# Performance work log

Hardware: AMD Instinct MI355X
Metric: run time of the kernel (lower is better)

## Reference

```python
import jax, jax.numpy as jnp
import numpy as np

HEAD_NUM = 16
MASK_FILL = 100000.0  # source uses +1e5 on masked entries (not -inf)


def setup_inputs() -> dict:
    key = jax.random.key(0)
    k1, k2, k3, k4, k5 = jax.random.split(key, 5)
    B, S, E = 2, 2048, 1024
    scale = 0.02
    return {
        "x": jax.random.normal(k1, (B, S, E), dtype=jnp.float32),
        "W_atten": jax.random.normal(k2, (E, 3 * E), dtype=jnp.float32) * scale,
        "b_atten": jax.random.normal(k3, (3 * E,), dtype=jnp.float32) * scale,
        "W_proj": jax.random.normal(k4, (E, E), dtype=jnp.float32) * scale,
        "b_proj": jax.random.normal(k5, (E,), dtype=jnp.float32) * scale,
    }


def reference(x, W_atten, b_atten, W_proj, b_proj):
    B, S, E = x.shape
    H = HEAD_NUM
    hd = E // H
    # QKV projection: [B, S, 3E]
    qkv = x @ W_atten + b_atten
    # reshape [B, S, H, 3*hd] -> [B, H, S, 3*hd], chunk into q,k,v [B,H,S,hd]
    qkv = jnp.transpose(qkv.reshape(B, S, H, 3 * hd), (0, 2, 1, 3))
    q, k, v = jnp.split(qkv, 3, axis=-1)
    # raw scores, NO 1/sqrt(dk) scaling (faithful to source)
    w = jnp.einsum("bhqd,bhkd->bhqk", q, k)
    # causal mask applied as w*mask + (1-mask)*1e5 (faithful to source)
    mask = jnp.tril(jnp.ones((S, S), dtype=w.dtype))
    w = w * mask + (1.0 - mask) * MASK_FILL
    # softmax over dim=1 == HEAD axis (faithful to source quirk)
    w = jax.nn.softmax(w, axis=1)
    # attn_drop: identity in eval mode
    a = jnp.einsum("bhqk,bhkd->bhqd", w, v)  # [B,H,S,hd]
    a = jnp.transpose(a, (0, 2, 1, 3)).reshape(B, S, E)
    h = a @ W_proj + b_proj
    # resi_drop: identity in eval mode
    return h
```

## Files before the change

### kernel.cpp

```cpp
#include <hip/hip_runtime.h>

#define DI __device__ __forceinline__

typedef __attribute__((ext_vector_type(8))) short s16x8;
typedef __attribute__((ext_vector_type(4))) short s16x4;
typedef __attribute__((ext_vector_type(4))) float f32x4;

DI unsigned short f2bf(float f){
  unsigned u = __float_as_uint(f);
  u = (u + 0x7FFFu + ((u >> 16) & 1u)) >> 16;
  return (unsigned short)u;
}
DI float bf2f(unsigned short h){
  return __uint_as_float(((unsigned)h) << 16);
}

DI void gll16(const void* g, void* l){
  __builtin_amdgcn_global_load_lds((const __attribute__((address_space(1))) void*)g,
                                   (__attribute__((address_space(3))) void*)l, 16, 0, 0);
}

__global__ void cvt_kernel(const float* __restrict__ in, unsigned short* __restrict__ out, int n8){
  int i = blockIdx.x * blockDim.x + threadIdx.x;
  if (i >= n8) return;
  const float4* p = (const float4*)in + (size_t)i * 2;
  float4 a = p[0], b = p[1];
  s16x8 o;
  o[0] = (short)f2bf(a.x); o[1] = (short)f2bf(a.y); o[2] = (short)f2bf(a.z); o[3] = (short)f2bf(a.w);
  o[4] = (short)f2bf(b.x); o[5] = (short)f2bf(b.y); o[6] = (short)f2bf(b.z); o[7] = (short)f2bf(b.w);
  ((s16x8*)out)[i] = o;
}

__global__ void transpose_cvt(const float* __restrict__ in, unsigned short* __restrict__ out, int R, int C){
  __shared__ float t[32][33];
  int c0 = blockIdx.x * 32, r0 = blockIdx.y * 32;
  int tx = threadIdx.x, ty = threadIdx.y;
  #pragma unroll
  for (int i = 0; i < 4; i++)
    t[ty + i*8][tx] = in[(size_t)(r0 + ty + i*8) * C + c0 + tx];
  __syncthreads();
  #pragma unroll
  for (int i = 0; i < 4; i++)
    out[(size_t)(c0 + ty + i*8) * R + r0 + tx] = f2bf(t[tx][ty + i*8]);
}

template<int MODE, int BM>
__launch_bounds__(256)
__global__ void gemm_kernel(const unsigned short* __restrict__ A,
                            const unsigned short* __restrict__ Wt,
                            const float* __restrict__ bias,
                            int N,
                            unsigned short* __restrict__ qb,
                            unsigned short* __restrict__ kb,
                            unsigned short* __restrict__ vt,
                            float* __restrict__ out)
{
  constexpr int MI = BM / 32;
  constexpr int AC = BM / 32;
  const int K = 1024;
  __shared__ unsigned short As[BM * 64];
  __shared__ unsigned short Bs[128 * 64];
  int m0 = blockIdx.y * BM, n0 = blockIdx.x * 128;
  int tid = threadIdx.x;
  int lane = tid & 63, w = tid >> 6;
  int row_l = lane & 15, kgrp = lane >> 4;
  int wm = (w >> 1) * (MI * 16), wn = (w & 1) * 64;

  const unsigned short* asrc[AC];
  const unsigned short* bsrc[4];
  int ldsoA[AC], ldsoB[4];
  int chunk = (lane & 7) ^ (lane >> 3);
  #pragma unroll
  for (int c4 = 0; c4 < AC; c4++){
    int r = c4*32 + w*8 + (lane >> 3);
    asrc[c4] = A + (size_t)(m0 + r) * K + chunk*8;
    ldsoA[c4] = (c4*32 + w*8) * 64;
  }
  #pragma unroll
  for (int c4 = 0; c4 < 4; c4++){
    int r = c4*32 + w*8 + (lane >> 3);
    bsrc[c4] = Wt + (size_t)(n0 + r) * K + chunk*8;
    ldsoB[c4] = (c4*32 + w*8) * 64;
  }
  int eA[MI], eB[4];
  #pragma unroll
  for (int i = 0; i < MI; i++){
    int ra = wm + i*16 + row_l;
    eA[i] = (ra*64 + kgrp*8) ^ ((ra & 7) << 3);
  }
  #pragma unroll
  for (int i = 0; i < 4; i++){
    int rb = wn + i*16 + row_l;
    eB[i] = (rb*64 + kgrp*8) ^ ((rb & 7) << 3);
  }

  f32x4 acc[MI][4];
  #pragma unroll
  for (int i = 0; i < MI; i++)
    #pragma unroll
    for (int j = 0; j < 4; j++)
      acc[i][j] = (f32x4){0.f, 0.f, 0.f, 0.f};

  for (int k0 = 0; k0 < K; k0 += 64){
    #pragma unroll
    for (int c4 = 0; c4 < AC; c4++)
      gll16(asrc[c4] + k0, (void*)(As + ldsoA[c4]));
    #pragma unroll
    for (int c4 = 0; c4 < 4; c4++)
      gll16(bsrc[c4] + k0, (void*)(Bs + ldsoB[c4]));
    __syncthreads();
    #pragma unroll
    for (int kc = 0; kc < 2; kc++){
      s16x8 af[MI], bfr[4];
      #pragma unroll
      for (int mi = 0; mi < MI; mi++)
        af[mi] = *(const s16x8*)&As[eA[mi] ^ (kc*32)];
      #pragma unroll
      for (int ni = 0; ni < 4; ni++)
        bfr[ni] = *(const s16x8*)&Bs[eB[ni] ^ (kc*32)];
      #pragma unroll
      for (int mi = 0; mi < MI; mi++)
        #pragma unroll
        for (int ni = 0; ni < 4; ni++)
          acc[mi][ni] = __builtin_amdgcn_mfma_f32_16x16x32_bf16(af[mi], bfr[ni], acc[mi][ni], 0, 0, 0);
    }
    __syncthreads();
  }

  #pragma unroll
  for (int mi = 0; mi < MI; mi++){
    #pragma unroll
    for (int ni = 0; ni < 4; ni++){
      #pragma unroll
      for (int j = 0; j < 4; j++){
        int gr = m0 + wm + mi*16 + kgrp*4 + j;
        int gc = n0 + wn + ni*16 + row_l;
        float v = acc[mi][ni][j] + bias[gc];
        if (MODE == 0){
          int h = gc / 192, cc = gc % 192;
          int b = gr >> 11, s = gr & 2047;
          unsigned short bv = f2bf(v);
          if (cc < 64){
            qb[(size_t)gr * 1024 + h*64 + cc] = bv;
          } else if (cc < 128){
            int d = cc - 64; int kt = s >> 6, kk = s & 63;
            kb[(size_t)((b*16 + h)*32 + kt) * 4096 + ((kk*64 + d) ^ ((kk & 7) << 3))] = bv;
          } else {
            int d = cc - 128; int kt = s >> 6, kk = s & 63;
            vt[(size_t)((b*16 + h)*32 + kt) * 4096 + ((d*64 + kk) ^ ((d & 7) << 3))] = bv;
          }
        } else {
          out[(size_t)gr * N + gc] = v;
        }
      }
    }
  }
}

__global__ void sufv_kernel(const unsigned short* __restrict__ vt, float* __restrict__ sufv){
  __shared__ float tot[4][64];
  int bh = blockIdx.x;
  int tid = threadIdx.x;
  int tq = tid >> 6, d = tid & 63;
  const unsigned short* base = vt + (size_t)bh * 32 * 4096;
  float s[8];
  float run = 0.f;
  for (int j = 7; j >= 0; j--){
    int t = tq*8 + j;
    float rs = 0.f;
    #pragma unroll
    for (int c = 0; c < 8; c++){
      int idx = (d*64 + c*8) ^ ((d & 7) << 3);
      s16x8 v = *(const s16x8*)&base[(size_t)t*4096 + idx];
      #pragma unroll
      for (int e = 0; e < 8; e++) rs += bf2f((unsigned short)v[e]);
    }
    run += rs; s[j] = run;
  }
  tot[tq][d] = run;
  __syncthreads();
  float carry = 0.f;
  for (int t2 = tq+1; t2 < 4; t2++) carry += tot[t2][d];
  #pragma unroll
  for (int j = 0; j < 8; j++)
    sufv[((size_t)bh*33 + tq*8 + j)*64 + d] = s[j] + carry;
  if (tid < 64) sufv[((size_t)bh*33 + 32)*64 + tid] = 0.f;
}

__launch_bounds__(256)
__global__ void dpass_kernel(const unsigned short* __restrict__ qbuf,
                             const unsigned short* __restrict__ kb,
                             float* __restrict__ invDQ)
{
  __shared__ unsigned short Kst[4][4096];
  int bid = blockIdx.x;
  int blk = (bid & 7) * 132 + (bid >> 3);
  int b = blk / 528, t = blk % 528;
  int kt = (int)(32.5f - sqrtf(1056.25f - 2.f*t));
  while (kt*(65-kt)/2 > t) kt--;
  while ((kt+1)*(64-kt)/2 <= t) kt++;
  int qt = kt + (t - kt*(65-kt)/2);

  int tid = threadIdx.x, lane = tid & 63, w = tid >> 6;
  int row_l = lane & 15, kgrp = lane >> 4;

  const unsigned short* ktb = kb + ((size_t)(b*16)*32 + kt) * 4096;
  int sgoff = (w*128 + lane)*8;

  auto stage = [&](int hh, int buf){
    const unsigned short* src = ktb + (size_t)hh * 131072;
    gll16(src + sgoff,       (void*)(&Kst[buf][0] + w*1024));
    gll16(src + sgoff + 512, (void*)(&Kst[buf][0] + w*1024 + 512));
  };

  int e0[4];
  #pragma unroll
  for (int ks = 0; ks < 4; ks++){
    int row = ks*16 + row_l;
    e0[ks] = (row*64 + kgrp*8) ^ ((row & 7) << 3);
  }

  stage(0, 0);
  stage(1, 1);

  f32x4 esum[4];
  #pragma unroll
  for (int ks = 0; ks < 4; ks++) esum[ks] = (f32x4){0.f,0.f,0.f,0.f};

  const unsigned short* qrow_p = qbuf + (size_t)(b*2048 + qt*64 + w*16 + row_l) * 1024;
  s16x8 qf0 = *(const s16x8*)&qrow_p[kgrp*8];
  s16x8 qf1 = *(const s16x8*)&qrow_p[32 + kgrp*8];

  for (int h = 0; h < 16; h++){
    s16x8 qn0, qn1;
    if (h < 15){
      qn0 = *(const s16x8*)&qrow_p[(h+1)*64 + kgrp*8];
      qn1 = *(const s16x8*)&qrow_p[(h+1)*64 + 32 + kgrp*8];
    }
    if (h + 2 < 16) stage(h+2, (h+2) & 3);
    __builtin_amdgcn_sched_barrier(0);
    if (h < 14)      asm volatile("s_waitcnt vmcnt(8)" ::: "memory");
    else if (h < 15) asm volatile("s_waitcnt vmcnt(6)" ::: "memory");
    else             asm volatile("s_waitcnt vmcnt(2)" ::: "memory");
    __builtin_amdgcn_sched_barrier(0);
    __builtin_amdgcn_s_barrier();
    __builtin_amdgcn_sched_barrier(0);

    const unsigned short* kl = &Kst[h & 3][0];
    #pragma unroll
    for (int ks = 0; ks < 4; ks++){
      s16x8 a0 = *(const s16x8*)&kl[e0[ks]];
      s16x8 a1 = *(const s16x8*)&kl[e0[ks] ^ 32];
      f32x4 sc = __builtin_amdgcn_mfma_f32_16x16x32_bf16(a0, qf0, (f32x4){0.f,0.f,0.f,0.f}, 0, 0, 0);
      sc = __builtin_amdgcn_mfma_f32_16x16x32_bf16(a1, qf1, sc, 0, 0, 0);
      #pragma unroll
      for (int j = 0; j < 4; j++) esum[ks][j] += __expf(sc[j]);
    }
    if (h < 15){ qf0 = qn0; qf1 = qn1; }
  }

  int qcol = qt*64 + w*16 + row_l;
  float* dst = invDQ + (size_t)b*4194304 + (size_t)qcol*2048 + kt*64 + kgrp*4;
  #pragma unroll
  for (int ks = 0; ks < 4; ks++){
    f32x4 rv;
    #pragma unroll
    for (int j = 0; j < 4; j++) rv[j] = 1.f / esum[ks][j];
    *(f32x4*)&dst[ks*16] = rv;
  }
}

__launch_bounds__(256)
__global__ void pv_kernel(const unsigned short* __restrict__ qbuf,
                          const unsigned short* __restrict__ kb,
                          const unsigned short* __restrict__ vt,
                          const float* __restrict__ invDQ,
                          const float* __restrict__ sufv,
                          unsigned short* __restrict__ ab,
                          float* __restrict__ pb)
{
  __shared__ unsigned short Kst[2][4096];
  __shared__ unsigned short Vst[2][4096];
  __shared__ unsigned short Wsh[4][1152];

  int blk = ((blockIdx.x & 7) << 7) + (blockIdx.x >> 3);
  int b = blk >> 9;
  int r = blk & 511;
  int h = r >> 5;
  int r2 = r & 31;
  int i = r2 >> 1, half = r2 & 1;
  int qsm = i, qbig = 31 - i;

  int tid = threadIdx.x, lane = tid & 63, w = tid >> 6;
  int row_l = lane & 15, kgrp = lane >> 4;

  const unsigned short* KT = kb + (size_t)((b*16 + h)*32) * 4096;
  const unsigned short* VT = vt + (size_t)((b*16 + h)*32) * 4096;
  int sgoff = (w*128 + lane)*8;
  unsigned short* Wsw = &Wsh[w][0];

  int eK[4];
  #pragma unroll
  for (int ks = 0; ks < 4; ks++){
    int row = ks*16 + row_l;
    eK[ks] = (row*64 + kgrp*8) ^ ((row & 7) << 3);
  }

  auto stage = [&](int kt, int buf){
    gll16(KT + (size_t)kt*4096 + sgoff,       (void*)(&Kst[buf][0] + w*1024));
    gll16(KT + (size_t)kt*4096 + sgoff + 512, (void*)(&Kst[buf][0] + w*1024 + 512));
    gll16(VT + (size_t)kt*4096 + sgoff,       (void*)(&Vst[buf][0] + w*1024));
    gll16(VT + (size_t)kt*4096 + sgoff + 512, (void*)(&Vst[buf][0] + w*1024 + 512));
  };

  auto run = [&](int qt, int k0t, int k1t, int mode){
    int q0 = qt * 64;
    int qv = q0 + w*16 + row_l;
    const unsigned short* qrow_p = qbuf + (size_t)(b*2048 + qv) * 1024 + h*64;
    s16x8 qf0 = *(const s16x8*)&qrow_p[kgrp*8];
    s16x8 qf1 = *(const s16x8*)&qrow_p[32 + kgrp*8];
    const float* ivrow = invDQ + (size_t)b*4194304 + (size_t)qv*2048 + kgrp*4;

    f32x4 pvv[4];
    #pragma unroll
    for (int d = 0; d < 4; d++) pvv[d] = (f32x4){0.f,0.f,0.f,0.f};

    __syncthreads();
    stage(k0t, 0);
    f32x4 inxt[4];
    #pragma unroll
    for (int ks = 0; ks < 4; ks++) inxt[ks] = *(const f32x4*)&ivrow[k0t*64 + ks*16];

    for (int kt = k0t; kt < k1t; kt++){
      int bufc = (kt - k0t) & 1;
      bool nx = (kt + 1 < k1t);
      __builtin_amdgcn_s_barrier();
      if (nx) stage(kt+1, bufc ^ 1);
      f32x4 icur[4];
      #pragma unroll
      for (int ks = 0; ks < 4; ks++) icur[ks] = inxt[ks];
      if (nx){
        #pragma unroll
        for (int ks = 0; ks < 4; ks++) inxt[ks] = *(const f32x4*)&ivrow[(kt+1)*64 + ks*16];
      }
      __builtin_amdgcn_sched_barrier(0);
      if (nx) asm volatile("s_waitcnt vmcnt(12)" ::: "memory");
      else    asm volatile("s_waitcnt vmcnt(4)" ::: "memory");
      __builtin_amdgcn_sched_barrier(0);
      __builtin_amdgcn_s_barrier();
      __builtin_amdgcn_sched_barrier(0);

      const unsigned short* kl = &Kst[bufc][0];
      const unsigned short* vl = &Vst[bufc][0];
      f32x4 sc[4];
      #pragma unroll
      for (int ks = 0; ks < 4; ks++){
        s16x8 a0 = *(const s16x8*)&kl[eK[ks]];
        s16x8 a1 = *(const s16x8*)&kl[eK[ks] ^ 32];
        sc[ks] = __builtin_amdgcn_mfma_f32_16x16x32_bf16(a0, qf0, (f32x4){0.f,0.f,0.f,0.f}, 0, 0, 0);
        sc[ks] = __builtin_amdgcn_mfma_f32_16x16x32_bf16(a1, qf1, sc[ks], 0, 0, 0);
      }
      int kbase = kt*64 + kgrp*4;
      #pragma unroll
      for (int ks = 0; ks < 4; ks++){
        #pragma unroll
        for (int j = 0; j < 4; j++){
          float e = __expf(sc[ks][j]);
          sc[ks][j] = (kbase + ks*16 + j > qv) ? 0.0625f : e * icur[ks][j];
        }
        unsigned lo, hi;
        asm("v_cvt_pk_bf16_f32 %0, %1, %2" : "=v"(lo) : "v"(sc[ks][0]), "v"(sc[ks][1]));
        asm("v_cvt_pk_bf16_f32 %0, %1, %2" : "=v"(hi) : "v"(sc[ks][2]), "v"(sc[ks][3]));
        uint2 pk2; pk2.x = lo; pk2.y = hi;
        *(uint2*)&Wsw[row_l*72 + ks*16 + kgrp*4] = pk2;
      }
      #pragma unroll
      for (int kc = 0; kc < 2; kc++){
        s16x8 af = *(const s16x8*)&Wsw[row_l*72 + kc*32 + kgrp*8];
        #pragma unroll
        for (int dq = 0; dq < 4; dq++){
          s16x8 vf = *(const s16x8*)&vl[eK[dq] ^ (kc*32)];
          pvv[dq] = __builtin_amdgcn_mfma_f32_16x16x32_bf16(af, vf, pvv[dq], 0, 0, 0);
        }
      }
    }

    if (mode == 0){
      int tsuf = qt + 1;
      #pragma unroll
      for (int dq = 0; dq < 4; dq++){
        int d = dq*16 + row_l;
        float suf = sufv[((size_t)(b*16 + h)*33 + tsuf)*64 + d];
        #pragma unroll
        for (int j = 0; j < 4; j++){
          int qo = q0 + w*16 + kgrp*4 + j;
          ab[(size_t)(b*2048 + qo)*1024 + h*64 + d] = f2bf(pvv[dq][j] + 0.0625f * suf);
        }
      }
    } else {
      float* pr = pb + ((size_t)((b*16 + h)*16 + i)*2 + (mode - 1)) * 4096;
      #pragma unroll
      for (int dq = 0; dq < 4; dq++){
        int d = dq*16 + row_l;
        #pragma unroll
        for (int j = 0; j < 4; j++)
          pr[(w*16 + kgrp*4 + j)*64 + d] = pvv[dq][j];
      }
    }
  };

  if (half == 0){
    run(qsm, 0, i + 1, 0);
    run(qbig, 0, 16 - i, 1);
  } else {
    run(qbig, 16 - i, 32 - i, 2);
  }
}

__global__ void reduce_kernel(const float* __restrict__ pb,
                              const float* __restrict__ sufv,
                              unsigned short* __restrict__ ab)
{
  int blk = blockIdx.x;
  int b = blk >> 8, rr = blk & 255;
  int h = rr >> 4, i = rr & 15;
  int qbig = 31 - i, tsuf = 32 - i;
  int t = threadIdx.x;
  int q = t >> 2, dbase = (t & 3) * 16;
  const float* p0 = pb + ((size_t)((b*16 + h)*16 + i)*2 + 0)*4096 + q*64 + dbase;
  const float* p1 = p0 + 4096;
  const float* sf = sufv + ((size_t)(b*16 + h)*33 + tsuf)*64 + dbase;
  unsigned short* op = ab + (size_t)(b*2048 + qbig*64 + q)*1024 + h*64 + dbase;
  #pragma unroll
  for (int e = 0; e < 4; e++){
    float4 a = *(const float4*)(p0 + e*4);
    float4 bb = *(const float4*)(p1 + e*4);
    float4 s = *(const float4*)(sf + e*4);
    unsigned short o[4];
    o[0] = f2bf(a.x + bb.x + 0.0625f * s.x);
    o[1] = f2bf(a.y + bb.y + 0.0625f * s.y);
    o[2] = f2bf(a.z + bb.z + 0.0625f * s.z);
    o[3] = f2bf(a.w + bb.w + 0.0625f * s.w);
    *(s16x4*)(op + e*4) = *(s16x4*)o;
  }
}

extern "C" void kernel_launch(void* const* d_in, const int* in_sizes, int n_in,
                              void* d_out, int out_size, void* d_ws, size_t ws_size,
                              hipStream_t stream) {
  (void)in_sizes; (void)n_in; (void)out_size; (void)ws_size;
  const float* x  = (const float*)d_in[0];
  const float* Wa = (const float*)d_in[1];
  const float* ba = (const float*)d_in[2];
  const float* Wp = (const float*)d_in[3];
  const float* bp = (const float*)d_in[4];
  float* out = (float*)d_out;

  char* ws = (char*)d_ws;
  size_t off = 0;
  auto alloc = [&](size_t bytes) -> void* {
    void* p = ws + off;
    off += (bytes + 255) & ~(size_t)255;
    return p;
  };
  float* pbuf          = (float*)alloc((size_t)16*1024*1024);
  unsigned short* xb   = (unsigned short*)((char*)pbuf);
  unsigned short* WaT  = (unsigned short*)((char*)pbuf + (size_t)4096*1024*2);
  unsigned short* WpT  = (unsigned short*)alloc((size_t)1024*1024*2);
  unsigned short* qbuf = (unsigned short*)alloc((size_t)4096*1024*2);
  unsigned short* ktile= (unsigned short*)alloc((size_t)4096*1024*2);
  unsigned short* vtile= (unsigned short*)alloc((size_t)4096*1024*2);
  unsigned short* abuf = (unsigned short*)alloc((size_t)4096*1024*2);
  float* invDQ         = (float*)alloc((size_t)2*2048*2048*4);
  float* sufv          = (float*)alloc((size_t)32*33*64*4);

  cvt_kernel<<<2048, 256, 0, stream>>>(x, xb, 4096*1024/8);
  transpose_cvt<<<dim3(3072/32, 1024/32), dim3(32, 8), 0, stream>>>(Wa, WaT, 1024, 3072);
  transpose_cvt<<<dim3(1024/32, 1024/32), dim3(32, 8), 0, stream>>>(Wp, WpT, 1024, 1024);

  gemm_kernel<0,128><<<dim3(24, 32), 256, 0, stream>>>(xb, WaT, ba, 3072, qbuf, ktile, vtile, nullptr);

  sufv_kernel<<<32, 256, 0, stream>>>(vtile, sufv);

  dpass_kernel<<<1056, 256, 0, stream>>>(qbuf, ktile, invDQ);

  pv_kernel<<<1024, 256, 0, stream>>>(qbuf, ktile, vtile, invDQ, sufv, abuf, pbuf);

  reduce_kernel<<<512, 256, 0, stream>>>(pbuf, sufv, abuf);

  gemm_kernel<1,64><<<dim3(1024/128, 4096/64), 256, 0, stream>>>(abuf, WpT, bp, 1024, nullptr, nullptr, nullptr, out);
}
```

Before: 182.8 us.

## Store inverse denominators in bf16, use exp2 with prescaled Q, deepen K prefetch

Q is prescaled by log2(e) in the QKV GEMM epilogue so both attention kernels can use the raw v_exp_f32 (exp2) instruction instead of __expf. The per-(q,k) inverse-denominator buffer goes from fp32 to bf16, halving its write and read traffic. pv_kernel gains a triple-buffered K stage with split K/V staging and a two-step-ahead prefetch of the inverse values, skips causal masking on tiles off the diagonal, adds s_setprio around the MFMA blocks, and sets a 3-blocks-per-SM launch bound. The bf16 inverse factors lose precision, and the extra LDS and register limit may affect occupancy.

```diff
diff --git a/kernel.cpp b/kernel.cpp
--- a/kernel.cpp
+++ b/kernel.cpp
@@ -14,11 +14,14 @@
 DI float bf2f(unsigned short h){
   return __uint_as_float(((unsigned)h) << 16);
 }
+DI float exp2i(float x){ float r; asm("v_exp_f32 %0, %1" : "=v"(r) : "v"(x)); return r; }
 
 DI void gll16(const void* g, void* l){
   __builtin_amdgcn_global_load_lds((const __attribute__((address_space(1))) void*)g,
                                    (__attribute__((address_space(3))) void*)l, 16, 0, 0);
 }
+
+#define VMCNT(n) asm volatile("s_waitcnt vmcnt(" #n ")" ::: "memory")
 
 __global__ void cvt_kernel(const float* __restrict__ in, unsigned short* __restrict__ out, int n8){
   int i = blockIdx.x * blockDim.x + threadIdx.x;
@@ -139,15 +142,14 @@
         if (MODE == 0){
           int h = gc / 192, cc = gc % 192;
           int b = gr >> 11, s = gr & 2047;
-          unsigned short bv = f2bf(v);
           if (cc < 64){
-            qb[(size_t)gr * 1024 + h*64 + cc] = bv;
+            qb[(size_t)gr * 1024 + h*64 + cc] = f2bf(v * 1.44269504f);
           } else if (cc < 128){
             int d = cc - 64; int kt = s >> 6, kk = s & 63;
-            kb[(size_t)((b*16 + h)*32 + kt) * 4096 + ((kk*64 + d) ^ ((kk & 7) << 3))] = bv;
+            kb[(size_t)((b*16 + h)*32 + kt) * 4096 + ((kk*64 + d) ^ ((kk & 7) << 3))] = f2bf(v);
           } else {
             int d = cc - 128; int kt = s >> 6, kk = s & 63;
-            vt[(size_t)((b*16 + h)*32 + kt) * 4096 + ((d*64 + kk) ^ ((d & 7) << 3))] = bv;
+            vt[(size_t)((b*16 + h)*32 + kt) * 4096 + ((d*64 + kk) ^ ((d & 7) << 3))] = f2bf(v);
           }
         } else {
           out[(size_t)gr * N + gc] = v;
@@ -190,7 +192,7 @@
 __launch_bounds__(256)
 __global__ void dpass_kernel(const unsigned short* __restrict__ qbuf,
                              const unsigned short* __restrict__ kb,
-                             float* __restrict__ invDQ)
+                             unsigned short* __restrict__ invb)
 {
   __shared__ unsigned short Kst[4][4096];
   int bid = blockIdx.x;
@@ -239,9 +241,9 @@
     }
     if (h + 2 < 16) stage(h+2, (h+2) & 3);
     __builtin_amdgcn_sched_barrier(0);
-    if (h < 14)      asm volatile("s_waitcnt vmcnt(8)" ::: "memory");
-    else if (h < 15) asm volatile("s_waitcnt vmcnt(6)" ::: "memory");
-    else             asm volatile("s_waitcnt vmcnt(2)" ::: "memory");
+    if (h < 14)      VMCNT(8);
+    else if (h < 15) VMCNT(6);
+    else             VMCNT(2);
     __builtin_amdgcn_sched_barrier(0);
     __builtin_amdgcn_s_barrier();
     __builtin_amdgcn_sched_barrier(0);
@@ -254,32 +256,35 @@
       f32x4 sc = __builtin_amdgcn_mfma_f32_16x16x32_bf16(a0, qf0, (f32x4){0.f,0.f,0.f,0.f}, 0, 0, 0);
       sc = __builtin_amdgcn_mfma_f32_16x16x32_bf16(a1, qf1, sc, 0, 0, 0);
       #pragma unroll
-      for (int j = 0; j < 4; j++) esum[ks][j] += __expf(sc[j]);
+      for (int j = 0; j < 4; j++) esum[ks][j] += exp2i(sc[j]);
     }
     if (h < 15){ qf0 = qn0; qf1 = qn1; }
   }
 
   int qcol = qt*64 + w*16 + row_l;
-  float* dst = invDQ + (size_t)b*4194304 + (size_t)qcol*2048 + kt*64 + kgrp*4;
+  unsigned short* dst = invb + (size_t)b*4194304 + (size_t)qcol*2048 + kt*64 + kgrp*4;
   #pragma unroll
   for (int ks = 0; ks < 4; ks++){
-    f32x4 rv;
-    #pragma unroll
-    for (int j = 0; j < 4; j++) rv[j] = 1.f / esum[ks][j];
-    *(f32x4*)&dst[ks*16] = rv;
-  }
-}
-
-__launch_bounds__(256)
+    float r0 = 1.f/esum[ks][0], r1 = 1.f/esum[ks][1];
+    float r2 = 1.f/esum[ks][2], r3 = 1.f/esum[ks][3];
+    unsigned lo, hi;
+    asm("v_cvt_pk_bf16_f32 %0, %1, %2" : "=v"(lo) : "v"(r0), "v"(r1));
+    asm("v_cvt_pk_bf16_f32 %0, %1, %2" : "=v"(hi) : "v"(r2), "v"(r3));
+    uint2 pk; pk.x = lo; pk.y = hi;
+    *(uint2*)&dst[ks*16] = pk;
+  }
+}
+
+__launch_bounds__(256, 3)
 __global__ void pv_kernel(const unsigned short* __restrict__ qbuf,
                           const unsigned short* __restrict__ kb,
                           const unsigned short* __restrict__ vt,
-                          const float* __restrict__ invDQ,
+                          const unsigned short* __restrict__ invb,
                           const float* __restrict__ sufv,
                           unsigned short* __restrict__ ab,
                           float* __restrict__ pb)
 {
-  __shared__ unsigned short Kst[2][4096];
+  __shared__ unsigned short Kst[3][4096];
   __shared__ unsigned short Vst[2][4096];
   __shared__ unsigned short Wsh[4][1152];
 
@@ -306,9 +311,11 @@
     eK[ks] = (row*64 + kgrp*8) ^ ((row & 7) << 3);
   }
 
-  auto stage = [&](int kt, int buf){
+  auto stageK = [&](int kt, int buf){
     gll16(KT + (size_t)kt*4096 + sgoff,       (void*)(&Kst[buf][0] + w*1024));
     gll16(KT + (size_t)kt*4096 + sgoff + 512, (void*)(&Kst[buf][0] + w*1024 + 512));
+  };
+  auto stageV = [&](int kt, int buf){
     gll16(VT + (size_t)kt*4096 + sgoff,       (void*)(&Vst[buf][0] + w*1024));
     gll16(VT + (size_t)kt*4096 + sgoff + 512, (void*)(&Vst[buf][0] + w*1024 + 512));
   };
@@ -319,40 +326,54 @@
     const unsigned short* qrow_p = qbuf + (size_t)(b*2048 + qv) * 1024 + h*64;
     s16x8 qf0 = *(const s16x8*)&qrow_p[kgrp*8];
     s16x8 qf1 = *(const s16x8*)&qrow_p[32 + kgrp*8];
-    const float* ivrow = invDQ + (size_t)b*4194304 + (size_t)qv*2048 + kgrp*4;
+    const unsigned short* ivrow = invb + (size_t)b*4194304 + (size_t)qv*2048 + kgrp*4;
 
     f32x4 pvv[4];
     #pragma unroll
     for (int d = 0; d < 4; d++) pvv[d] = (f32x4){0.f,0.f,0.f,0.f};
 
     __syncthreads();
-    stage(k0t, 0);
-    f32x4 inxt[4];
-    #pragma unroll
-    for (int ks = 0; ks < 4; ks++) inxt[ks] = *(const f32x4*)&ivrow[k0t*64 + ks*16];
+    stageK(k0t, 0);
+    s16x4 i1[4], i2[4];
+    #pragma unroll
+    for (int ks = 0; ks < 4; ks++) i1[ks] = *(const s16x4*)&ivrow[k0t*64 + ks*16];
+    stageV(k0t, 0);
+    if (k0t + 1 < k1t){
+      stageK(k0t+1, 1);
+      #pragma unroll
+      for (int ks = 0; ks < 4; ks++) i2[ks] = *(const s16x4*)&ivrow[(k0t+1)*64 + ks*16];
+    }
 
     for (int kt = k0t; kt < k1t; kt++){
-      int bufc = (kt - k0t) & 1;
-      bool nx = (kt + 1 < k1t);
+      int bK = (kt - k0t) % 3, bV = (kt - k0t) & 1;
+      bool nx1 = (kt + 1 < k1t), nx2 = (kt + 2 < k1t);
+
       __builtin_amdgcn_s_barrier();
-      if (nx) stage(kt+1, bufc ^ 1);
-      f32x4 icur[4];
-      #pragma unroll
-      for (int ks = 0; ks < 4; ks++) icur[ks] = inxt[ks];
-      if (nx){
-        #pragma unroll
-        for (int ks = 0; ks < 4; ks++) inxt[ks] = *(const f32x4*)&ivrow[(kt+1)*64 + ks*16];
-      }
+      if (nx2) stageK(kt+2, (kt+2-k0t) % 3);
+      if (nx1) stageV(kt+1, bV ^ 1);
       __builtin_amdgcn_sched_barrier(0);
-      if (nx) asm volatile("s_waitcnt vmcnt(12)" ::: "memory");
-      else    asm volatile("s_waitcnt vmcnt(4)" ::: "memory");
+      int N = (kt == k0t) ? (nx1 ? (nx2 ? 10 : 8) : 0)
+                          : (nx2 ? 8 : (nx1 ? 6 : 0));
+      if (N == 10)     VMCNT(10);
+      else if (N == 8) VMCNT(8);
+      else if (N == 6) VMCNT(6);
+      else             VMCNT(0);
       __builtin_amdgcn_sched_barrier(0);
       __builtin_amdgcn_s_barrier();
       __builtin_amdgcn_sched_barrier(0);
 
-      const unsigned short* kl = &Kst[bufc][0];
-      const unsigned short* vl = &Vst[bufc][0];
+      s16x4 icur[4];
+      #pragma unroll
+      for (int ks = 0; ks < 4; ks++){ icur[ks] = i1[ks]; i1[ks] = i2[ks]; }
+      if (nx2){
+        #pragma unroll
+        for (int ks = 0; ks < 4; ks++) i2[ks] = *(const s16x4*)&ivrow[(kt+2)*64 + ks*16];
+      }
+
+      const unsigned short* kl = &Kst[bK][0];
+      const unsigned short* vl = &Vst[bV][0];
       f32x4 sc[4];
+      __builtin_amdgcn_s_setprio(1);
       #pragma unroll
       for (int ks = 0; ks < 4; ks++){
         s16x8 a0 = *(const s16x8*)&kl[eK[ks]];
@@ -360,20 +381,38 @@
         sc[ks] = __builtin_amdgcn_mfma_f32_16x16x32_bf16(a0, qf0, (f32x4){0.f,0.f,0.f,0.f}, 0, 0, 0);
         sc[ks] = __builtin_amdgcn_mfma_f32_16x16x32_bf16(a1, qf1, sc[ks], 0, 0, 0);
       }
-      int kbase = kt*64 + kgrp*4;
-      #pragma unroll
-      for (int ks = 0; ks < 4; ks++){
-        #pragma unroll
-        for (int j = 0; j < 4; j++){
-          float e = __expf(sc[ks][j]);
-          sc[ks][j] = (kbase + ks*16 + j > qv) ? 0.0625f : e * icur[ks][j];
+      __builtin_amdgcn_s_setprio(0);
+
+      if (kt == qt){
+        int kbase = kt*64 + kgrp*4;
+        #pragma unroll
+        for (int ks = 0; ks < 4; ks++){
+          #pragma unroll
+          for (int j = 0; j < 4; j++){
+            float wv = exp2i(sc[ks][j]) * bf2f((unsigned short)icur[ks][j]);
+            sc[ks][j] = (kbase + ks*16 + j > qv) ? 0.0625f : wv;
+          }
+          unsigned lo, hi;
+          asm("v_cvt_pk_bf16_f32 %0, %1, %2" : "=v"(lo) : "v"(sc[ks][0]), "v"(sc[ks][1]));
+          asm("v_cvt_pk_bf16_f32 %0, %1, %2" : "=v"(hi) : "v"(sc[ks][2]), "v"(sc[ks][3]));
+          uint2 pk2; pk2.x = lo; pk2.y = hi;
+          *(uint2*)&Wsw[row_l*72 + ks*16 + kgrp*4] = pk2;
         }
-        unsigned lo, hi;
-        asm("v_cvt_pk_bf16_f32 %0, %1, %2" : "=v"(lo) : "v"(sc[ks][0]), "v"(sc[ks][1]));
-        asm("v_cvt_pk_bf16_f32 %0, %1, %2" : "=v"(hi) : "v"(sc[ks][2]), "v"(sc[ks][3]));
-        uint2 pk2; pk2.x = lo; pk2.y = hi;
-        *(uint2*)&Wsw[row_l*72 + ks*16 + kgrp*4] = pk2;
-      }
+      } else {
+        #pragma unroll
+        for (int ks = 0; ks < 4; ks++){
+          #pragma unroll
+          for (int j = 0; j < 4; j++)
+            sc[ks][j] = exp2i(sc[ks][j]) * bf2f((unsigned short)icur[ks][j]);
+          unsigned lo, hi;
+          asm("v_cvt_pk_bf16_f32 %0, %1, %2" : "=v"(lo) : "v"(sc[ks][0]), "v"(sc[ks][1]));
+          asm("v_cvt_pk_bf16_f32 %0, %1, %2" : "=v"(hi) : "v"(sc[ks][2]), "v"(sc[ks][3]));
+          uint2 pk2; pk2.x = lo; pk2.y = hi;
+          *(uint2*)&Wsw[row_l*72 + ks*16 + kgrp*4] = pk2;
+        }
+      }
+
+      __builtin_amdgcn_s_setprio(1);
       #pragma unroll
       for (int kc = 0; kc < 2; kc++){
         s16x8 af = *(const s16x8*)&Wsw[row_l*72 + kc*32 + kgrp*8];
@@ -383,6 +422,7 @@
           pvv[dq] = __builtin_amdgcn_mfma_f32_16x16x32_bf16(af, vf, pvv[dq], 0, 0, 0);
         }
       }
+      __builtin_amdgcn_s_setprio(0);
     }
 
     if (mode == 0){
@@ -471,7 +511,7 @@
   unsigned short* ktile= (unsigned short*)alloc((size_t)4096*1024*2);
   unsigned short* vtile= (unsigned short*)alloc((size_t)4096*1024*2);
   unsigned short* abuf = (unsigned short*)alloc((size_t)4096*1024*2);
-  float* invDQ         = (float*)alloc((size_t)2*2048*2048*4);
+  unsigned short* invb = (unsigned short*)alloc((size_t)2*2048*2048*2);
   float* sufv          = (float*)alloc((size_t)32*33*64*4);
 
   cvt_kernel<<<2048, 256, 0, stream>>>(x, xb, 4096*1024/8);
@@ -482,9 +522,9 @@
 
   sufv_kernel<<<32, 256, 0, stream>>>(vtile, sufv);
 
-  dpass_kernel<<<1056, 256, 0, stream>>>(qbuf, ktile, invDQ);
-
-  pv_kernel<<<1024, 256, 0, stream>>>(qbuf, ktile, vtile, invDQ, sufv, abuf, pbuf);
+  dpass_kernel<<<1056, 256, 0, stream>>>(qbuf, ktile, invb);
+
+  pv_kernel<<<1024, 256, 0, stream>>>(qbuf, ktile, vtile, invb, sufv, abuf, pbuf);
 
   reduce_kernel<<<512, 256, 0, stream>>>(pbuf, sufv, abuf);
 
```

After: 178.7 us. -2.2%, faster.
